# Optimization experiments

Measured on AMD Instinct MI355X. Metric: run time of the kernel, lower is better.

The kernel has to match this reference:

```python
import jax, jax.numpy as jnp
import numpy as np

B, C, P, FD, D, H, W = 16, 6, 10, 256, 128, 128, 128


def setup_inputs() -> dict:
    key = jax.random.key(0)
    k0, k1, k2, k3, k4, k5 = jax.random.split(key, 6)
    return {
        "assp_features": jax.random.normal(k0, (B, FD, H, W), dtype=jnp.float32),
        "prototypes": jax.random.normal(k1, (B, C, P, FD), dtype=jnp.float32),
        # key conv (1x1): weight [128, featDim], bias [128]
        "Wk": jax.random.normal(k2, (D, FD), dtype=jnp.float32) * 0.05,
        "bk": jax.random.normal(k3, (D,), dtype=jnp.float32) * 0.05,
        # per-class query convs stacked: [num_classes, 128, featDim]
        "Wq": jax.random.normal(k4, (C, D, FD), dtype=jnp.float32) * 0.05,
        "bq": jax.random.normal(k5, (C, D), dtype=jnp.float32) * 0.05,
    }


def reference(assp_features, prototypes, Wk, bk, Wq, bq):
    b, fd, h, w = assp_features.shape
    # key: 1x1 conv == channel GEMM -> [B, D, H*W]
    key_out = jnp.einsum('df,bfhw->bdhw', Wk, assp_features) + bk[None, :, None, None]
    key_flat = key_out.reshape(b, key_out.shape[1], h * w)  # [B, D, HW]
    # all per-(class, prototype) query projections in one batched GEMM
    # q[b,c,p,d] = Wq[c] @ prototypes[b,c,p] + bq[c]
    q = jnp.einsum('cdf,bcpf->bcpd', Wq, prototypes) + bq[None, :, None, :]
    # similarity per (class, prototype): [B, C, P, HW] -> [B, C*P, H, W]
    sim = jnp.einsum('bcpd,bdn->bcpn', q, key_flat)
    c, p = q.shape[1], q.shape[2]
    sim = sim.reshape(b, c * p, h, w)
    weight = jax.nn.softmax(sim, axis=1)        # softmax over class*proto axis
    weight_max = jnp.max(weight, axis=1)        # [B, H, W]
    assp_weighted = assp_features * weight_max[:, None, :, :]
    # prototypesOut: list order is (i outer, j inner) == row-major flatten of [C, P]
    protos_out = q.reshape(b, c * p, -1)        # [B, C*P, 128]
    return (assp_weighted, protos_out)
```

## Files before the change

kernel.cpp:

```cpp
#include <hip/hip_runtime.h>

typedef _Float16 half8 __attribute__((ext_vector_type(8)));
typedef float f32x4 __attribute__((ext_vector_type(4)));

#define HW 16384
#define FDIM 256
#define DDIM 128

union H8 { half8 v; uint4 q; _Float16 h[8]; };
union H4 { uint2 q; _Float16 h[4]; };

__global__ __launch_bounds__(256) void prep_kernel(
    const float* __restrict__ proto, const float* __restrict__ Wk,
    const float* __restrict__ Wq, const float* __restrict__ bq,
    float* __restrict__ protos_out, _Float16* __restrict__ Wkf,
    _Float16* __restrict__ qf)
{
  const int bid = blockIdx.x, t = threadIdx.x;
  if (bid < 96) {
    const int b = bid / 6, c = bid % 6;
    __shared__ float protoS[10 * FDIM];
    const float* pbase = proto + (size_t)((b * 6 + c) * 10) * FDIM;
#pragma unroll
    for (int i = 0; i < 10; ++i) protoS[t + 256 * i] = pbase[t + 256 * i];
    __syncthreads();
#pragma unroll
    for (int i = 0; i < 5; ++i) {
      const int oid = t + 256 * i;
      const int p = oid >> 7, d = oid & 127;
      const float* wq = Wq + (size_t)(c * DDIM + d) * FDIM;
      float acc = bq[c * DDIM + d];
      for (int f = 0; f < FDIM; ++f) acc += wq[f] * protoS[p * FDIM + f];
      protos_out[((b * 6 + c) * 10 + p) * DDIM + d] = acc;
      const int cp = c * 10 + p;
      const int cpt = cp >> 4, lr = cp & 15, ks2 = d >> 5, lg = (d >> 3) & 3, j = d & 7;
      qf[((((b * 4 + cpt) * 4 + ks2) * 64) + lg * 16 + lr) * 8 + j] = (_Float16)acc;
    }
    if (c == 5) {
#pragma unroll
      for (int i = 0; i < 2; ++i) {
        const int zid = t + 256 * i;
        const int cp = 60 + (zid >> 7), d = zid & 127;
        const int cpt = cp >> 4, lr = cp & 15, ks2 = d >> 5, lg = (d >> 3) & 3, j = d & 7;
        qf[((((b * 4 + cpt) * 4 + ks2) * 64) + lg * 16 + lr) * 8 + j] = (_Float16)0.f;
      }
    }
  } else {
#pragma unroll
    for (int ii = 0; ii < 16; ++ii) {
      const int fl = t + 256 * ii;
      const int mt = fl >> 9, ks = (fl >> 6) & 7, l = fl & 63;
      const int d = mt * 16 + (l & 15), f0 = ks * 32 + ((l >> 4) << 3);
      H8 h;
#pragma unroll
      for (int j = 0; j < 8; ++j) h.h[j] = (_Float16)Wk[d * FDIM + f0 + j];
      *reinterpret_cast<uint4*>(Wkf + (size_t)fl * 8) = h.q;
    }
  }
}

#define XB_OFF 0
#define SIMK_OFF 16384
#define WM_OFF 24704
#define BKS_OFF 24832
#define SMEM_BYTES 25344

__global__ __launch_bounds__(256, 8) void fused_kernel(
    const float* __restrict__ assp, const float* __restrict__ bk,
    const _Float16* __restrict__ Wkf, const _Float16* __restrict__ qf,
    float* __restrict__ out)
{
  __shared__ __align__(16) char smem[SMEM_BYTES];
  const int t = threadIdx.x;
  const int b = blockIdx.x >> 9;
  const int tile = blockIdx.x & 511;
  const int pix = t & 31, cg = t >> 5;
  const int w = t >> 6, l = t & 63, l4 = l >> 4, lr = l & 15;
  const size_t gbase = (size_t)b * FDIM * HW + (size_t)tile * 32 + pix;

  if (t < 128) ((float*)(smem + BKS_OFF))[t] = bk[t];

#pragma unroll
  for (int g = 0; g < 4; ++g) {
    float x[8];
#pragma unroll
    for (int j = 0; j < 8; ++j) x[j] = assp[gbase + (size_t)(cg * 32 + g * 8 + j) * HW];
    H8 h;
#pragma unroll
    for (int j = 0; j < 8; ++j) h.h[j] = (_Float16)x[j];
    const int colb = (cg * 32 + g * 8) * 2;
    *reinterpret_cast<uint4*>(smem + XB_OFF + pix * 512 + (colb ^ ((pix & 7) << 4))) = h.q;
  }
  __syncthreads();

  f32x4 acc[2][2];
#pragma unroll
  for (int mt = 0; mt < 2; ++mt)
#pragma unroll
    for (int nt = 0; nt < 2; ++nt) acc[mt][nt] = (f32x4){0.f, 0.f, 0.f, 0.f};

#pragma unroll
  for (int ks = 0; ks < 8; ++ks) {
    const half8 a0 = *reinterpret_cast<const half8*>(Wkf + ((size_t)((w * 2 + 0) * 8 + ks) * 64 + l) * 8);
    const half8 a1 = *reinterpret_cast<const half8*>(Wkf + ((size_t)((w * 2 + 1) * 8 + ks) * 64 + l) * 8);
#pragma unroll
    for (int nt = 0; nt < 2; ++nt) {
      const int row = nt * 16 + lr;
      const half8 bb = *reinterpret_cast<const half8*>(
          smem + XB_OFF + row * 512 + ((ks * 64 + l4 * 16) ^ ((row & 7) << 4)));
      acc[0][nt] = __builtin_amdgcn_mfma_f32_16x16x32_f16(a0, bb, acc[0][nt], 0, 0, 0);
      acc[1][nt] = __builtin_amdgcn_mfma_f32_16x16x32_f16(a1, bb, acc[1][nt], 0, 0, 0);
    }
  }

  const float* bks = (const float*)(smem + BKS_OFF);
#pragma unroll
  for (int mt = 0; mt < 2; ++mt) {
    const int d0 = w * 32 + mt * 16 + l4 * 4;
    const float b0 = bks[d0], b1 = bks[d0 + 1], b2 = bks[d0 + 2], b3 = bks[d0 + 3];
#pragma unroll
    for (int nt = 0; nt < 2; ++nt) {
      H4 h;
      h.h[0] = (_Float16)(acc[mt][nt][0] + b0);
      h.h[1] = (_Float16)(acc[mt][nt][1] + b1);
      h.h[2] = (_Float16)(acc[mt][nt][2] + b2);
      h.h[3] = (_Float16)(acc[mt][nt][3] + b3);
      const int prow = nt * 16 + lr;
      *reinterpret_cast<uint2*>(smem + SIMK_OFF + prow * 256 + ((d0 * 2) ^ ((prow & 7) << 4))) = h.q;
    }
  }
  __syncthreads();

  f32x4 acc2[2];
#pragma unroll
  for (int nt = 0; nt < 2; ++nt) acc2[nt] = (f32x4){0.f, 0.f, 0.f, 0.f};
#pragma unroll
  for (int ks2 = 0; ks2 < 4; ++ks2) {
    const half8 a2 = *reinterpret_cast<const half8*>(qf + ((size_t)((b * 4 + w) * 4 + ks2) * 64 + l) * 8);
#pragma unroll
    for (int nt = 0; nt < 2; ++nt) {
      const int row = nt * 16 + lr;
      const half8 bb = *reinterpret_cast<const half8*>(
          smem + SIMK_OFF + row * 256 + ((ks2 * 64 + l4 * 16) ^ ((row & 7) << 4)));
      acc2[nt] = __builtin_amdgcn_mfma_f32_16x16x32_f16(a2, bb, acc2[nt], 0, 0, 0);
    }
  }
  __syncthreads();

  float* sim = (float*)(smem + SIMK_OFF);
#pragma unroll
  for (int nt = 0; nt < 2; ++nt) {
    const int spix = nt * 16 + lr;
#pragma unroll
    for (int r = 0; r < 4; ++r) sim[spix * 65 + (w * 16 + l4 * 4 + r)] = acc2[nt][r];
  }
  __syncthreads();

  if (t < 128) {
    const int spix = t >> 2, rq = t & 3;
    const float* srow = sim + spix * 65 + rq * 15;
    float m = -1e30f;
#pragma unroll
    for (int i = 0; i < 15; ++i) m = fmaxf(m, srow[i]);
    m = fmaxf(m, __shfl_xor(m, 1));
    m = fmaxf(m, __shfl_xor(m, 2));
    float s = 0.f;
#pragma unroll
    for (int i = 0; i < 15; ++i) s += expf(srow[i] - m);
    s += __shfl_xor(s, 1);
    s += __shfl_xor(s, 2);
    if (rq == 0) ((float*)(smem + WM_OFF))[spix] = 1.0f / s;
  }
  __syncthreads();

  const float wm = ((float*)(smem + WM_OFF))[pix];
#pragma unroll
  for (int g = 0; g < 4; ++g) {
    H8 h;
    const int colb = (cg * 32 + g * 8) * 2;
    h.q = *reinterpret_cast<const uint4*>(smem + XB_OFF + pix * 512 + (colb ^ ((pix & 7) << 4)));
#pragma unroll
    for (int j = 0; j < 8; ++j)
      __builtin_nontemporal_store((float)h.h[j] * wm,
                                  &out[gbase + (size_t)(cg * 32 + g * 8 + j) * HW]);
  }
}

extern "C" void kernel_launch(void* const* d_in, const int* in_sizes, int n_in,
                              void* d_out, int out_size, void* d_ws, size_t ws_size,
                              hipStream_t stream) {
  const float* assp  = (const float*)d_in[0];
  const float* proto = (const float*)d_in[1];
  const float* Wk    = (const float*)d_in[2];
  const float* bk    = (const float*)d_in[3];
  const float* Wq    = (const float*)d_in[4];
  const float* bq    = (const float*)d_in[5];
  float* out = (float*)d_out;
  float* protos_out = out + (size_t)16 * FDIM * HW;

  _Float16* Wkf = (_Float16*)d_ws;
  _Float16* qf  = Wkf + 32768;

  prep_kernel<<<97, 256, 0, stream>>>(proto, Wk, Wq, bq, protos_out, Wkf, qf);
  fused_kernel<<<16 * 512, 256, 0, stream>>>(assp, bk, Wkf, qf, out);
}
```

Baseline: 147.8 us.

## Double pixel tile to 64 per block with 512 threads and swizzle block order

Each block now handles 64 pixels with 512 threads (8 waves) instead of 32 pixels with 256 threads, and the work split across waves is reorganised: each wave computes 16 key rows over 4 pixel subtiles, and the similarity GEMM is split by prototype tile and pixel half. Softmax now uses 8 lanes per pixel with masking of the padded rows. Block indices are swizzled so consecutive blocks go to different batches/tiles. The aim is fewer blocks and wider 256-byte coalesced row segments per channel, at the cost of doubled LDS per block and possibly lower occupancy.

Measured after the change: 164.4 us. 11.3% more time.

```diff
diff --git a/kernel.cpp b/kernel.cpp
--- a/kernel.cpp
+++ b/kernel.cpp
@@ -60,23 +60,24 @@
 }
 
 #define XB_OFF 0
-#define SIMK_OFF 16384
-#define WM_OFF 24704
-#define BKS_OFF 24832
-#define SMEM_BYTES 25344
-
-__global__ __launch_bounds__(256, 8) void fused_kernel(
+#define SIMK_OFF 32768
+#define WM_OFF 49408
+#define BKS_OFF 49664
+#define SMEM_BYTES 50176
+
+__global__ __launch_bounds__(512) void fused_kernel(
     const float* __restrict__ assp, const float* __restrict__ bk,
     const _Float16* __restrict__ Wkf, const _Float16* __restrict__ qf,
     float* __restrict__ out)
 {
   __shared__ __align__(16) char smem[SMEM_BYTES];
   const int t = threadIdx.x;
-  const int b = blockIdx.x >> 9;
-  const int tile = blockIdx.x & 511;
-  const int pix = t & 31, cg = t >> 5;
-  const int w = t >> 6, l = t & 63, l4 = l >> 4, lr = l & 15;
-  const size_t gbase = (size_t)b * FDIM * HW + (size_t)tile * 32 + pix;
+  const int swz = (blockIdx.x & 7) * 512 + (blockIdx.x >> 3);
+  const int b = swz >> 8;
+  const int tile = swz & 255;
+  const int pix = t & 63, w = t >> 6;
+  const int l = t & 63, l4 = l >> 4, lr = l & 15;
+  const size_t gbase = (size_t)b * FDIM * HW + (size_t)tile * 64 + pix;
 
   if (t < 128) ((float*)(smem + BKS_OFF))[t] = bk[t];
 
@@ -84,62 +85,58 @@
   for (int g = 0; g < 4; ++g) {
     float x[8];
 #pragma unroll
-    for (int j = 0; j < 8; ++j) x[j] = assp[gbase + (size_t)(cg * 32 + g * 8 + j) * HW];
+    for (int j = 0; j < 8; ++j) x[j] = assp[gbase + (size_t)(w * 32 + g * 8 + j) * HW];
     H8 h;
 #pragma unroll
     for (int j = 0; j < 8; ++j) h.h[j] = (_Float16)x[j];
-    const int colb = (cg * 32 + g * 8) * 2;
+    const int colb = (w * 32 + g * 8) * 2;
     *reinterpret_cast<uint4*>(smem + XB_OFF + pix * 512 + (colb ^ ((pix & 7) << 4))) = h.q;
   }
   __syncthreads();
 
-  f32x4 acc[2][2];
-#pragma unroll
-  for (int mt = 0; mt < 2; ++mt)
-#pragma unroll
-    for (int nt = 0; nt < 2; ++nt) acc[mt][nt] = (f32x4){0.f, 0.f, 0.f, 0.f};
+  f32x4 acc[4];
+#pragma unroll
+  for (int nt = 0; nt < 4; ++nt) acc[nt] = (f32x4){0.f, 0.f, 0.f, 0.f};
 
 #pragma unroll
   for (int ks = 0; ks < 8; ++ks) {
-    const half8 a0 = *reinterpret_cast<const half8*>(Wkf + ((size_t)((w * 2 + 0) * 8 + ks) * 64 + l) * 8);
-    const half8 a1 = *reinterpret_cast<const half8*>(Wkf + ((size_t)((w * 2 + 1) * 8 + ks) * 64 + l) * 8);
-#pragma unroll
-    for (int nt = 0; nt < 2; ++nt) {
+    const half8 a0 = *reinterpret_cast<const half8*>(Wkf + ((size_t)(w * 8 + ks) * 64 + l) * 8);
+#pragma unroll
+    for (int nt = 0; nt < 4; ++nt) {
       const int row = nt * 16 + lr;
       const half8 bb = *reinterpret_cast<const half8*>(
           smem + XB_OFF + row * 512 + ((ks * 64 + l4 * 16) ^ ((row & 7) << 4)));
-      acc[0][nt] = __builtin_amdgcn_mfma_f32_16x16x32_f16(a0, bb, acc[0][nt], 0, 0, 0);
-      acc[1][nt] = __builtin_amdgcn_mfma_f32_16x16x32_f16(a1, bb, acc[1][nt], 0, 0, 0);
+      acc[nt] = __builtin_amdgcn_mfma_f32_16x16x32_f16(a0, bb, acc[nt], 0, 0, 0);
     }
   }
 
   const float* bks = (const float*)(smem + BKS_OFF);
-#pragma unroll
-  for (int mt = 0; mt < 2; ++mt) {
-    const int d0 = w * 32 + mt * 16 + l4 * 4;
+  {
+    const int d0 = w * 16 + l4 * 4;
     const float b0 = bks[d0], b1 = bks[d0 + 1], b2 = bks[d0 + 2], b3 = bks[d0 + 3];
 #pragma unroll
-    for (int nt = 0; nt < 2; ++nt) {
+    for (int nt = 0; nt < 4; ++nt) {
       H4 h;
-      h.h[0] = (_Float16)(acc[mt][nt][0] + b0);
-      h.h[1] = (_Float16)(acc[mt][nt][1] + b1);
-      h.h[2] = (_Float16)(acc[mt][nt][2] + b2);
-      h.h[3] = (_Float16)(acc[mt][nt][3] + b3);
+      h.h[0] = (_Float16)(acc[nt][0] + b0);
+      h.h[1] = (_Float16)(acc[nt][1] + b1);
+      h.h[2] = (_Float16)(acc[nt][2] + b2);
+      h.h[3] = (_Float16)(acc[nt][3] + b3);
       const int prow = nt * 16 + lr;
       *reinterpret_cast<uint2*>(smem + SIMK_OFF + prow * 256 + ((d0 * 2) ^ ((prow & 7) << 4))) = h.q;
     }
   }
   __syncthreads();
 
+  const int cpt = w >> 1, nh = w & 1;
   f32x4 acc2[2];
 #pragma unroll
   for (int nt = 0; nt < 2; ++nt) acc2[nt] = (f32x4){0.f, 0.f, 0.f, 0.f};
 #pragma unroll
   for (int ks2 = 0; ks2 < 4; ++ks2) {
-    const half8 a2 = *reinterpret_cast<const half8*>(qf + ((size_t)((b * 4 + w) * 4 + ks2) * 64 + l) * 8);
+    const half8 a2 = *reinterpret_cast<const half8*>(qf + ((size_t)((b * 4 + cpt) * 4 + ks2) * 64 + l) * 8);
 #pragma unroll
     for (int nt = 0; nt < 2; ++nt) {
-      const int row = nt * 16 + lr;
+      const int row = (nh * 2 + nt) * 16 + lr;
       const half8 bb = *reinterpret_cast<const half8*>(
           smem + SIMK_OFF + row * 256 + ((ks2 * 64 + l4 * 16) ^ ((row & 7) << 4)));
       acc2[nt] = __builtin_amdgcn_mfma_f32_16x16x32_f16(a2, bb, acc2[nt], 0, 0, 0);
@@ -150,25 +147,27 @@
   float* sim = (float*)(smem + SIMK_OFF);
 #pragma unroll
   for (int nt = 0; nt < 2; ++nt) {
-    const int spix = nt * 16 + lr;
-#pragma unroll
-    for (int r = 0; r < 4; ++r) sim[spix * 65 + (w * 16 + l4 * 4 + r)] = acc2[nt][r];
-  }
-  __syncthreads();
-
-  if (t < 128) {
-    const int spix = t >> 2, rq = t & 3;
-    const float* srow = sim + spix * 65 + rq * 15;
+    const int spix = (nh * 2 + nt) * 16 + lr;
+#pragma unroll
+    for (int r = 0; r < 4; ++r) sim[spix * 65 + (cpt * 16 + l4 * 4 + r)] = acc2[nt][r];
+  }
+  __syncthreads();
+
+  {
+    const int spix = t >> 3, rq = t & 7;
+    const float* srow = sim + spix * 65 + rq * 8;
     float m = -1e30f;
 #pragma unroll
-    for (int i = 0; i < 15; ++i) m = fmaxf(m, srow[i]);
+    for (int i = 0; i < 8; ++i) if (rq * 8 + i < 60) m = fmaxf(m, srow[i]);
     m = fmaxf(m, __shfl_xor(m, 1));
     m = fmaxf(m, __shfl_xor(m, 2));
+    m = fmaxf(m, __shfl_xor(m, 4));
     float s = 0.f;
 #pragma unroll
-    for (int i = 0; i < 15; ++i) s += expf(srow[i] - m);
+    for (int i = 0; i < 8; ++i) if (rq * 8 + i < 60) s += expf(srow[i] - m);
     s += __shfl_xor(s, 1);
     s += __shfl_xor(s, 2);
+    s += __shfl_xor(s, 4);
     if (rq == 0) ((float*)(smem + WM_OFF))[spix] = 1.0f / s;
   }
   __syncthreads();
@@ -177,12 +176,12 @@
 #pragma unroll
   for (int g = 0; g < 4; ++g) {
     H8 h;
-    const int colb = (cg * 32 + g * 8) * 2;
+    const int colb = (w * 32 + g * 8) * 2;
     h.q = *reinterpret_cast<const uint4*>(smem + XB_OFF + pix * 512 + (colb ^ ((pix & 7) << 4)));
 #pragma unroll
     for (int j = 0; j < 8; ++j)
       __builtin_nontemporal_store((float)h.h[j] * wm,
-                                  &out[gbase + (size_t)(cg * 32 + g * 8 + j) * HW]);
+                                  &out[gbase + (size_t)(w * 32 + g * 8 + j) * HW]);
   }
 }
 
@@ -202,5 +201,5 @@
   _Float16* qf  = Wkf + 32768;
 
   prep_kernel<<<97, 256, 0, stream>>>(proto, Wk, Wq, bq, protos_out, Wkf, qf);
-  fused_kernel<<<16 * 512, 256, 0, stream>>>(assp, bk, Wkf, qf, out);
+  fused_kernel<<<4096, 512, 0, stream>>>(assp, bk, Wkf, qf, out);
 }
```

## Fold key projection into query weights to collapse two GEMMs into one

Applied to the files above, without the earlier changes.

Precomputes per-batch combined weights Wc = q·Wk (and q·bk bias) in a new prep kernel, so the fused kernel does a single 64x256 GEMM against the features instead of computing the 128-dim key and then a second GEMM. This removes the intermediate key tile, one MFMA stage and two barriers per block. It adds a small extra kernel launch and a serial dependency on protos_out, and also drops the occupancy hint in launch bounds.

Result: slower. 152.3 us (+3.1%).

```diff
diff --git a/kernel.cpp b/kernel.cpp
--- a/kernel.cpp
+++ b/kernel.cpp
@@ -8,67 +8,78 @@
 #define DDIM 128
 
 union H8 { half8 v; uint4 q; _Float16 h[8]; };
-union H4 { uint2 q; _Float16 h[4]; };
 
 __global__ __launch_bounds__(256) void prep_kernel(
-    const float* __restrict__ proto, const float* __restrict__ Wk,
-    const float* __restrict__ Wq, const float* __restrict__ bq,
-    float* __restrict__ protos_out, _Float16* __restrict__ Wkf,
-    _Float16* __restrict__ qf)
+    const float* __restrict__ proto, const float* __restrict__ Wq,
+    const float* __restrict__ bq, float* __restrict__ protos_out)
 {
   const int bid = blockIdx.x, t = threadIdx.x;
-  if (bid < 96) {
-    const int b = bid / 6, c = bid % 6;
-    __shared__ float protoS[10 * FDIM];
-    const float* pbase = proto + (size_t)((b * 6 + c) * 10) * FDIM;
+  const int b = bid / 6, c = bid % 6;
+  __shared__ float protoS[10 * FDIM];
+  const float* pbase = proto + (size_t)((b * 6 + c) * 10) * FDIM;
 #pragma unroll
-    for (int i = 0; i < 10; ++i) protoS[t + 256 * i] = pbase[t + 256 * i];
-    __syncthreads();
+  for (int i = 0; i < 10; ++i) protoS[t + 256 * i] = pbase[t + 256 * i];
+  __syncthreads();
 #pragma unroll
-    for (int i = 0; i < 5; ++i) {
-      const int oid = t + 256 * i;
-      const int p = oid >> 7, d = oid & 127;
-      const float* wq = Wq + (size_t)(c * DDIM + d) * FDIM;
-      float acc = bq[c * DDIM + d];
-      for (int f = 0; f < FDIM; ++f) acc += wq[f] * protoS[p * FDIM + f];
-      protos_out[((b * 6 + c) * 10 + p) * DDIM + d] = acc;
-      const int cp = c * 10 + p;
-      const int cpt = cp >> 4, lr = cp & 15, ks2 = d >> 5, lg = (d >> 3) & 3, j = d & 7;
-      qf[((((b * 4 + cpt) * 4 + ks2) * 64) + lg * 16 + lr) * 8 + j] = (_Float16)acc;
-    }
-    if (c == 5) {
+  for (int i = 0; i < 5; ++i) {
+    const int oid = t + 256 * i;
+    const int p = oid >> 7, d = oid & 127;
+    const float* wq = Wq + (size_t)(c * DDIM + d) * FDIM;
+    float acc = bq[c * DDIM + d];
+    for (int f = 0; f < FDIM; ++f) acc += wq[f] * protoS[p * FDIM + f];
+    protos_out[((b * 6 + c) * 10 + p) * DDIM + d] = acc;
+  }
+}
+
+__global__ __launch_bounds__(256) void prep2_kernel(
+    const float* __restrict__ q ,
+    const float* __restrict__ Wk, const float* __restrict__ bk,
+    _Float16* __restrict__ Wcf, float* __restrict__ qbk)
+{
+  __shared__ float qS[16][128];
+  __shared__ float bkS[128];
+  const int t = threadIdx.x;
+  const int b = blockIdx.x >> 2, cpt = blockIdx.x & 3;
 #pragma unroll
-      for (int i = 0; i < 2; ++i) {
-        const int zid = t + 256 * i;
-        const int cp = 60 + (zid >> 7), d = zid & 127;
-        const int cpt = cp >> 4, lr = cp & 15, ks2 = d >> 5, lg = (d >> 3) & 3, j = d & 7;
-        qf[((((b * 4 + cpt) * 4 + ks2) * 64) + lg * 16 + lr) * 8 + j] = (_Float16)0.f;
-      }
-    }
-  } else {
+  for (int i = 0; i < 8; ++i) {
+    const int idx = t + 256 * i;
+    const int row = idx >> 7, d = idx & 127;
+    const int cp = cpt * 16 + row;
+    qS[row][d] = (cp < 60) ? q[((size_t)b * 60 + cp) * DDIM + d] : 0.f;
+  }
+  if (t < 128) bkS[t] = bk[t];
+  __syncthreads();
+
+  float acc[16];
 #pragma unroll
-    for (int ii = 0; ii < 16; ++ii) {
-      const int fl = t + 256 * ii;
-      const int mt = fl >> 9, ks = (fl >> 6) & 7, l = fl & 63;
-      const int d = mt * 16 + (l & 15), f0 = ks * 32 + ((l >> 4) << 3);
-      H8 h;
+  for (int i = 0; i < 16; ++i) acc[i] = 0.f;
+  const int f = t;
+  for (int d = 0; d < 128; ++d) {
+    const float wv = Wk[d * FDIM + f];
 #pragma unroll
-      for (int j = 0; j < 8; ++j) h.h[j] = (_Float16)Wk[d * FDIM + f0 + j];
-      *reinterpret_cast<uint4*>(Wkf + (size_t)fl * 8) = h.q;
-    }
+    for (int i = 0; i < 16; ++i) acc[i] += qS[i][d] * wv;
+  }
+  const int ks = f >> 5, lg = (f >> 3) & 3, j = f & 7;
+#pragma unroll
+  for (int i = 0; i < 16; ++i)
+    Wcf[((((size_t)(b * 4 + cpt) * 8 + ks) * 64) + lg * 16 + i) * 8 + j] = (_Float16)acc[i];
+
+  if (t < 16) {
+    float s = 0.f;
+    for (int d = 0; d < 128; ++d) s += qS[t][d] * bkS[d];
+    qbk[b * 64 + cpt * 16 + t] = s;
   }
 }
 
 #define XB_OFF 0
-#define SIMK_OFF 16384
-#define WM_OFF 24704
-#define BKS_OFF 24832
-#define SMEM_BYTES 25344
+#define SIM_OFF 16384
+#define QBK_OFF 24704
+#define WM_OFF 24960
+#define SMEM_BYTES 25088
 
-__global__ __launch_bounds__(256, 8) void fused_kernel(
-    const float* __restrict__ assp, const float* __restrict__ bk,
-    const _Float16* __restrict__ Wkf, const _Float16* __restrict__ qf,
-    float* __restrict__ out)
+__global__ __launch_bounds__(256) void fused_kernel(
+    const float* __restrict__ assp, const _Float16* __restrict__ Wcf,
+    const float* __restrict__ qbk, float* __restrict__ out)
 {
   __shared__ __align__(16) char smem[SMEM_BYTES];
   const int t = threadIdx.x;
@@ -78,7 +89,7 @@
   const int w = t >> 6, l = t & 63, l4 = l >> 4, lr = l & 15;
   const size_t gbase = (size_t)b * FDIM * HW + (size_t)tile * 32 + pix;
 
-  if (t < 128) ((float*)(smem + BKS_OFF))[t] = bk[t];
+  if (t < 64) ((float*)(smem + QBK_OFF))[t] = qbk[b * 64 + t];
 
 #pragma unroll
   for (int g = 0; g < 4; ++g) {
@@ -93,66 +104,29 @@
   }
   __syncthreads();
 
-  f32x4 acc[2][2];
+  f32x4 acc2[2];
 #pragma unroll
-  for (int mt = 0; mt < 2; ++mt)
-#pragma unroll
-    for (int nt = 0; nt < 2; ++nt) acc[mt][nt] = (f32x4){0.f, 0.f, 0.f, 0.f};
-
+  for (int nt = 0; nt < 2; ++nt) acc2[nt] = (f32x4){0.f, 0.f, 0.f, 0.f};
 #pragma unroll
   for (int ks = 0; ks < 8; ++ks) {
-    const half8 a0 = *reinterpret_cast<const half8*>(Wkf + ((size_t)((w * 2 + 0) * 8 + ks) * 64 + l) * 8);
-    const half8 a1 = *reinterpret_cast<const half8*>(Wkf + ((size_t)((w * 2 + 1) * 8 + ks) * 64 + l) * 8);
+    const half8 a2 = *reinterpret_cast<const half8*>(Wcf + ((size_t)((b * 4 + w) * 8 + ks) * 64 + l) * 8);
 #pragma unroll
     for (int nt = 0; nt < 2; ++nt) {
       const int row = nt * 16 + lr;
       const half8 bb = *reinterpret_cast<const half8*>(
           smem + XB_OFF + row * 512 + ((ks * 64 + l4 * 16) ^ ((row & 7) << 4)));
-      acc[0][nt] = __builtin_amdgcn_mfma_f32_16x16x32_f16(a0, bb, acc[0][nt], 0, 0, 0);
-      acc[1][nt] = __builtin_amdgcn_mfma_f32_16x16x32_f16(a1, bb, acc[1][nt], 0, 0, 0);
+      acc2[nt] = __builtin_amdgcn_mfma_f32_16x16x32_f16(a2, bb, acc2[nt], 0, 0, 0);
     }
   }
 
-  const float* bks = (const float*)(smem + BKS_OFF);
-#pragma unroll
-  for (int mt = 0; mt < 2; ++mt) {
-    const int d0 = w * 32 + mt * 16 + l4 * 4;
-    const float b0 = bks[d0], b1 = bks[d0 + 1], b2 = bks[d0 + 2], b3 = bks[d0 + 3];
-#pragma unroll
-    for (int nt = 0; nt < 2; ++nt) {
-      H4 h;
-      h.h[0] = (_Float16)(acc[mt][nt][0] + b0);
-      h.h[1] = (_Float16)(acc[mt][nt][1] + b1);
-      h.h[2] = (_Float16)(acc[mt][nt][2] + b2);
-      h.h[3] = (_Float16)(acc[mt][nt][3] + b3);
-      const int prow = nt * 16 + lr;
-      *reinterpret_cast<uint2*>(smem + SIMK_OFF + prow * 256 + ((d0 * 2) ^ ((prow & 7) << 4))) = h.q;
-    }
-  }
-  __syncthreads();
-
-  f32x4 acc2[2];
-#pragma unroll
-  for (int nt = 0; nt < 2; ++nt) acc2[nt] = (f32x4){0.f, 0.f, 0.f, 0.f};
-#pragma unroll
-  for (int ks2 = 0; ks2 < 4; ++ks2) {
-    const half8 a2 = *reinterpret_cast<const half8*>(qf + ((size_t)((b * 4 + w) * 4 + ks2) * 64 + l) * 8);
-#pragma unroll
-    for (int nt = 0; nt < 2; ++nt) {
-      const int row = nt * 16 + lr;
-      const half8 bb = *reinterpret_cast<const half8*>(
-          smem + SIMK_OFF + row * 256 + ((ks2 * 64 + l4 * 16) ^ ((row & 7) << 4)));
-      acc2[nt] = __builtin_amdgcn_mfma_f32_16x16x32_f16(a2, bb, acc2[nt], 0, 0, 0);
-    }
-  }
-  __syncthreads();
-
-  float* sim = (float*)(smem + SIMK_OFF);
+  float* sim = (float*)(smem + SIM_OFF);
+  const float* qbkS = (const float*)(smem + QBK_OFF);
 #pragma unroll
   for (int nt = 0; nt < 2; ++nt) {
     const int spix = nt * 16 + lr;
 #pragma unroll
-    for (int r = 0; r < 4; ++r) sim[spix * 65 + (w * 16 + l4 * 4 + r)] = acc2[nt][r];
+    for (int r = 0; r < 4; ++r)
+      sim[spix * 65 + (w * 16 + l4 * 4 + r)] = acc2[nt][r] + qbkS[w * 16 + l4 * 4 + r];
   }
   __syncthreads();
 
@@ -198,9 +172,10 @@
   float* out = (float*)d_out;
   float* protos_out = out + (size_t)16 * FDIM * HW;
 
-  _Float16* Wkf = (_Float16*)d_ws;
-  _Float16* qf  = Wkf + 32768;
+  _Float16* Wcf = (_Float16*)d_ws;
+  float* qbk    = (float*)(Wcf + 262144);
 
-  prep_kernel<<<97, 256, 0, stream>>>(proto, Wk, Wq, bq, protos_out, Wkf, qf);
-  fused_kernel<<<16 * 512, 256, 0, stream>>>(assp, bk, Wkf, qf, out);
+  prep_kernel<<<96, 256, 0, stream>>>(proto, Wq, bq, protos_out);
+  prep2_kernel<<<64, 256, 0, stream>>>(protos_out, Wk, bk, Wcf, qbk);
+  fused_kernel<<<16 * 512, 256, 0, stream>>>(assp, Wcf, qbk, out);
 }
```
